# Kernel tuning notes

Measured on AMD Instinct MI355X. Metric: run time of the kernel, lower is better.

Reference implementation:

```python
import jax, jax.numpy as jnp
import numpy as np

B, N, D_IN, D_HID = 8, 2048, 5, 32

def setup_inputs() -> dict:
    key = jax.random.key(0)
    k1, k2, k3, k4 = jax.random.split(key, 4)
    s = jax.random.normal(k1, (B, N, D_IN), dtype=jnp.float32)
    Gmat = jax.random.uniform(k2, (B, N, N), dtype=jnp.float32)
    Qweight = jax.random.normal(k3, (D_IN, D_HID), dtype=jnp.float32)
    Kweight = jax.random.normal(k4, (D_IN, D_HID), dtype=jnp.float32)
    return {"s": s, "Gmat": Gmat, "Qweight": Qweight, "Kweight": Kweight}

def reference(s, Gmat, Qweight, Kweight):
    # s: [B, N, 5]; Gmat: [B, N, N] (or [N, N], broadcastable)
    if Gmat.ndim == 2:
        Gmat = Gmat[None]
    q = jnp.einsum('bnd,dm->bnm', s, Qweight)   # [B, N, 32]
    k = jnp.einsum('bnd,dm->bnm', s, Kweight)   # [B, N, 32]
    att = jnp.square(jnp.einsum('bnm,bjm->bnj', q, k)) * Gmat  # [B, N, N]
    att = att / (jnp.sum(att, axis=2, keepdims=True) + 0.001)
    return att
```

## Files before the change

kernel.cpp:

```cpp
#include <hip/hip_runtime.h>

constexpr int Bc   = 8;
constexpr int Nc   = 2048;
constexpr int DIN  = 5;
constexpr int DHID = 32;

typedef float vf4 __attribute__((ext_vector_type(4)));

__global__ __launch_bounds__(256) void u_precompute(
    const float* __restrict__ s, const float* __restrict__ Qw,
    const float* __restrict__ Kw, float* __restrict__ u)
{
    __shared__ float Msh[DIN * DIN];
    const int tid = threadIdx.x;
    if (tid < DIN * DIN) {
        const int d = tid / DIN, e = tid % DIN;
        float acc = 0.f;
        #pragma unroll
        for (int m = 0; m < DHID; ++m)
            acc = fmaf(Qw[d * DHID + m], Kw[e * DHID + m], acc);
        Msh[tid] = acc;
    }
    __syncthreads();
    const int g = blockIdx.x * 256 + tid;
    if (g >= Bc * Nc) return;
    const int b = g >> 11;
    const int j = g & (Nc - 1);
    float sv[DIN];
    #pragma unroll
    for (int e = 0; e < DIN; ++e) sv[e] = s[(size_t)g * DIN + e];
    #pragma unroll
    for (int d = 0; d < DIN; ++d) {
        float acc = 0.f;
        #pragma unroll
        for (int e = 0; e < DIN; ++e) acc = fmaf(Msh[d * DIN + e], sv[e], acc);
        u[((size_t)b * DIN + d) * Nc + j] = acc;
    }
}

__global__ __launch_bounds__(256) void att_wave_row(
    const float* __restrict__ s, const float* __restrict__ G,
    const float* __restrict__ u, float* __restrict__ out, long gbs)
{
    const int tid  = threadIdx.x;
    const int lane = tid & 63;
    const int wid  = tid >> 6;
    const int row  = blockIdx.x * 4 + wid;
    const int b    = row >> 11;
    const int i    = row & (Nc - 1);

    const float* gRow = G + (size_t)b * gbs + (size_t)i * Nc;
    const float* ub   = u + (size_t)b * DIN * Nc;
    float*       oRow = out + (size_t)row * Nc;

    float si[DIN];
    #pragma unroll
    for (int d = 0; d < DIN; ++d) si[d] = s[(size_t)row * DIN + d];

    float4 g4[8];
    #pragma unroll
    for (int k = 0; k < 8; ++k)
        g4[k] = *reinterpret_cast<const float4*>(gRow + k * 256 + lane * 4);

    float a[8][4];
    float psum = 0.f;
    #pragma unroll
    for (int k = 0; k < 8; ++k) {
        const int j0 = k * 256 + lane * 4;
        float vx = 0.f, vy = 0.f, vz = 0.f, vw = 0.f;
        #pragma unroll
        for (int d = 0; d < DIN; ++d) {
            const float4 u4 = *reinterpret_cast<const float4*>(ub + (size_t)d * Nc + j0);
            vx = fmaf(si[d], u4.x, vx);
            vy = fmaf(si[d], u4.y, vy);
            vz = fmaf(si[d], u4.z, vz);
            vw = fmaf(si[d], u4.w, vw);
        }
        a[k][0] = vx * vx * g4[k].x;
        a[k][1] = vy * vy * g4[k].y;
        a[k][2] = vz * vz * g4[k].z;
        a[k][3] = vw * vw * g4[k].w;
        psum += (a[k][0] + a[k][1]) + (a[k][2] + a[k][3]);
    }

    #pragma unroll
    for (int off = 32; off > 0; off >>= 1)
        psum += __shfl_xor(psum, off, 64);
    const float inv = 1.0f / (psum + 0.001f);

    #pragma unroll
    for (int k = 0; k < 8; ++k) {
        const int j0 = k * 256 + lane * 4;
        vf4 o;
        o.x = a[k][0] * inv;
        o.y = a[k][1] * inv;
        o.z = a[k][2] * inv;
        o.w = a[k][3] * inv;
        __builtin_nontemporal_store(o, reinterpret_cast<vf4*>(oRow + j0));
    }
}

__global__ __launch_bounds__(256) void att_row_direct(
    const float* __restrict__ s, const float* __restrict__ G,
    const float* __restrict__ Qw, const float* __restrict__ Kw,
    float* __restrict__ out, long gbs)
{
    __shared__ float Msh[DIN * DIN];
    __shared__ float wpart[4];
    const int tid = threadIdx.x;
    if (tid < DIN * DIN) {
        const int d = tid / DIN, e = tid % DIN;
        float acc = 0.f;
        #pragma unroll
        for (int m = 0; m < DHID; ++m)
            acc = fmaf(Qw[d * DHID + m], Kw[e * DHID + m], acc);
        Msh[tid] = acc;
    }
    __syncthreads();

    const int row = blockIdx.x;
    const int b   = row >> 11;
    const int i   = row & (Nc - 1);

    float w[DIN];
    {
        float si[DIN];
        #pragma unroll
        for (int e = 0; e < DIN; ++e) si[e] = s[(size_t)row * DIN + e];
        #pragma unroll
        for (int d = 0; d < DIN; ++d) {
            float acc = 0.f;
            #pragma unroll
            for (int e = 0; e < DIN; ++e) acc = fmaf(si[e], Msh[e * DIN + d], acc);
            w[d] = acc;
        }
    }

    const float* gRow = G + (size_t)b * gbs + (size_t)i * Nc;
    const float* sb   = s + (size_t)b * Nc * DIN;
    float*       oRow = out + (size_t)row * Nc;

    float a[2][4];
    float lsum = 0.f;
    #pragma unroll
    for (int it = 0; it < 2; ++it) {
        const int j0 = it * 1024 + tid * 4;
        const float4 g4 = *reinterpret_cast<const float4*>(gRow + j0);
        float v[4];
        #pragma unroll
        for (int c = 0; c < 4; ++c) {
            const float* sj = sb + (size_t)(j0 + c) * DIN;
            float acc = 0.f;
            #pragma unroll
            for (int d = 0; d < DIN; ++d) acc = fmaf(w[d], sj[d], acc);
            v[c] = acc;
        }
        a[it][0] = v[0] * v[0] * g4.x;
        a[it][1] = v[1] * v[1] * g4.y;
        a[it][2] = v[2] * v[2] * g4.z;
        a[it][3] = v[3] * v[3] * g4.w;
        lsum += (a[it][0] + a[it][1]) + (a[it][2] + a[it][3]);
    }

    #pragma unroll
    for (int off = 32; off > 0; off >>= 1)
        lsum += __shfl_xor(lsum, off, 64);
    if ((tid & 63) == 0) wpart[tid >> 6] = lsum;
    __syncthreads();
    const float total = (wpart[0] + wpart[1]) + (wpart[2] + wpart[3]);
    const float inv = 1.0f / (total + 0.001f);

    #pragma unroll
    for (int it = 0; it < 2; ++it) {
        const int j0 = it * 1024 + tid * 4;
        vf4 o;
        o.x = a[it][0] * inv;
        o.y = a[it][1] * inv;
        o.z = a[it][2] * inv;
        o.w = a[it][3] * inv;
        __builtin_nontemporal_store(o, reinterpret_cast<vf4*>(oRow + j0));
    }
}

extern "C" void kernel_launch(void* const* d_in, const int* in_sizes, int n_in,
                              void* d_out, int out_size, void* d_ws, size_t ws_size,
                              hipStream_t stream)
{
    const float* s  = (const float*)d_in[0];
    const float* G  = (const float*)d_in[1];
    const float* Qw = (const float*)d_in[2];
    const float* Kw = (const float*)d_in[3];
    float* out = (float*)d_out;

    const long gbs = (in_sizes[1] == Nc * Nc) ? 0L : (long)Nc * Nc;

    const size_t uBytes = (size_t)Bc * DIN * Nc * sizeof(float);
    if (ws_size >= uBytes) {
        float* u = (float*)d_ws;
        u_precompute<<<(Bc * Nc + 255) / 256, 256, 0, stream>>>(s, Qw, Kw, u);
        att_wave_row<<<(Bc * Nc) / 4, 256, 0, stream>>>(s, G, u, out, gbs);
    } else {
        att_row_direct<<<Bc * Nc, 256, 0, stream>>>(s, G, Qw, Kw, out, gbs);
    }
}
```

Before: 251.6 us.

## Split row normalization into atomic-sum pass and separate grid-stride write pass

Replaces the one-wave-per-row fused kernel with two grid-stride kernels. The first accumulates per-row sums via wave reductions and atomicAdd into a zeroed workspace. The second recomputes attention values and scales them by the inverse sum. This removes the per-thread register arrays and improves occupancy, but G is now read twice and a zeroing kernel plus atomics are added.

New measurement: 291.1 us. 1.16x slower.

```diff
diff --git a/kernel.cpp b/kernel.cpp
--- a/kernel.cpp
+++ b/kernel.cpp
@@ -1,9 +1,11 @@
 #include <hip/hip_runtime.h>
 
-constexpr int Bc   = 8;
-constexpr int Nc   = 2048;
-constexpr int DIN  = 5;
-constexpr int DHID = 32;
+constexpr int  Bc    = 8;
+constexpr int  Nc    = 2048;
+constexpr int  DIN   = 5;
+constexpr int  DHID  = 32;
+constexpr int  NROWS = Bc * Nc;
+constexpr long NF4   = (long)Bc * Nc * (Nc / 4);
 
 typedef float vf4 __attribute__((ext_vector_type(4)));
 
@@ -23,7 +25,7 @@
     }
     __syncthreads();
     const int g = blockIdx.x * 256 + tid;
-    if (g >= Bc * Nc) return;
+    if (g >= NROWS) return;
     const int b = g >> 11;
     const int j = g & (Nc - 1);
     float sv[DIN];
@@ -38,65 +40,82 @@
     }
 }
 
-__global__ __launch_bounds__(256) void att_wave_row(
+__global__ __launch_bounds__(256) void zero_sums(float* __restrict__ sums)
+{
+    const int i = blockIdx.x * 256 + threadIdx.x;
+    if (i < NROWS) sums[i] = 0.f;
+}
+
+__global__ __launch_bounds__(256) void pass1_sums(
     const float* __restrict__ s, const float* __restrict__ G,
-    const float* __restrict__ u, float* __restrict__ out, long gbs)
-{
-    const int tid  = threadIdx.x;
-    const int lane = tid & 63;
-    const int wid  = tid >> 6;
-    const int row  = blockIdx.x * 4 + wid;
-    const int b    = row >> 11;
-    const int i    = row & (Nc - 1);
-
-    const float* gRow = G + (size_t)b * gbs + (size_t)i * Nc;
-    const float* ub   = u + (size_t)b * DIN * Nc;
-    float*       oRow = out + (size_t)row * Nc;
-
-    float si[DIN];
-    #pragma unroll
-    for (int d = 0; d < DIN; ++d) si[d] = s[(size_t)row * DIN + d];
-
-    float4 g4[8];
-    #pragma unroll
-    for (int k = 0; k < 8; ++k)
-        g4[k] = *reinterpret_cast<const float4*>(gRow + k * 256 + lane * 4);
-
-    float a[8][4];
-    float psum = 0.f;
-    #pragma unroll
-    for (int k = 0; k < 8; ++k) {
-        const int j0 = k * 256 + lane * 4;
+    const float* __restrict__ u, float* __restrict__ sums, long gbs)
+{
+    const long stride = (long)gridDim.x * 256;
+    const int  lane   = threadIdx.x & 63;
+    for (long f = (long)blockIdx.x * 256 + threadIdx.x; f < NF4; f += stride) {
+        const int r  = (int)(f >> 9);
+        const int b  = r >> 11;
+        const int i  = r & (Nc - 1);
+        const int j0 = ((int)f & 511) * 4;
+
+        const float4 g4 = *reinterpret_cast<const float4*>(
+            G + (size_t)b * gbs + (size_t)i * Nc + j0);
+
+        const float* sp = s + (size_t)r * DIN;
+        const float* ub = u + (size_t)b * DIN * Nc;
         float vx = 0.f, vy = 0.f, vz = 0.f, vw = 0.f;
         #pragma unroll
         for (int d = 0; d < DIN; ++d) {
+            const float sd = sp[d];
             const float4 u4 = *reinterpret_cast<const float4*>(ub + (size_t)d * Nc + j0);
-            vx = fmaf(si[d], u4.x, vx);
-            vy = fmaf(si[d], u4.y, vy);
-            vz = fmaf(si[d], u4.z, vz);
-            vw = fmaf(si[d], u4.w, vw);
-        }
-        a[k][0] = vx * vx * g4[k].x;
-        a[k][1] = vy * vy * g4[k].y;
-        a[k][2] = vz * vz * g4[k].z;
-        a[k][3] = vw * vw * g4[k].w;
-        psum += (a[k][0] + a[k][1]) + (a[k][2] + a[k][3]);
-    }
-
-    #pragma unroll
-    for (int off = 32; off > 0; off >>= 1)
-        psum += __shfl_xor(psum, off, 64);
-    const float inv = 1.0f / (psum + 0.001f);
-
-    #pragma unroll
-    for (int k = 0; k < 8; ++k) {
-        const int j0 = k * 256 + lane * 4;
+            vx = fmaf(sd, u4.x, vx);
+            vy = fmaf(sd, u4.y, vy);
+            vz = fmaf(sd, u4.z, vz);
+            vw = fmaf(sd, u4.w, vw);
+        }
+        float p = vx * vx * g4.x + vy * vy * g4.y + vz * vz * g4.z + vw * vw * g4.w;
+
+        #pragma unroll
+        for (int off = 32; off > 0; off >>= 1)
+            p += __shfl_xor(p, off, 64);
+        if (lane == 0) atomicAdd(&sums[r], p);
+    }
+}
+
+__global__ __launch_bounds__(256) void pass2_write(
+    const float* __restrict__ s, const float* __restrict__ G,
+    const float* __restrict__ u, const float* __restrict__ sums,
+    float* __restrict__ out, long gbs)
+{
+    const long stride = (long)gridDim.x * 256;
+    for (long f = (long)blockIdx.x * 256 + threadIdx.x; f < NF4; f += stride) {
+        const int r  = (int)(f >> 9);
+        const int b  = r >> 11;
+        const int i  = r & (Nc - 1);
+        const int j0 = ((int)f & 511) * 4;
+
+        const float4 g4 = *reinterpret_cast<const float4*>(
+            G + (size_t)b * gbs + (size_t)i * Nc + j0);
+
+        const float* sp = s + (size_t)r * DIN;
+        const float* ub = u + (size_t)b * DIN * Nc;
+        float vx = 0.f, vy = 0.f, vz = 0.f, vw = 0.f;
+        #pragma unroll
+        for (int d = 0; d < DIN; ++d) {
+            const float sd = sp[d];
+            const float4 u4 = *reinterpret_cast<const float4*>(ub + (size_t)d * Nc + j0);
+            vx = fmaf(sd, u4.x, vx);
+            vy = fmaf(sd, u4.y, vy);
+            vz = fmaf(sd, u4.z, vz);
+            vw = fmaf(sd, u4.w, vw);
+        }
+        const float inv = 1.0f / (sums[r] + 0.001f);
         vf4 o;
-        o.x = a[k][0] * inv;
-        o.y = a[k][1] * inv;
-        o.z = a[k][2] * inv;
-        o.w = a[k][3] * inv;
-        __builtin_nontemporal_store(o, reinterpret_cast<vf4*>(oRow + j0));
+        o.x = vx * vx * g4.x * inv;
+        o.y = vy * vy * g4.y * inv;
+        o.z = vz * vz * g4.z * inv;
+        o.w = vw * vw * g4.w * inv;
+        __builtin_nontemporal_store(o, reinterpret_cast<vf4*>(out + (f << 2)));
     }
 }
 
@@ -194,12 +213,18 @@
 
     const long gbs = (in_sizes[1] == Nc * Nc) ? 0L : (long)Nc * Nc;
 
-    const size_t uBytes = (size_t)Bc * DIN * Nc * sizeof(float);
-    if (ws_size >= uBytes) {
-        float* u = (float*)d_ws;
-        u_precompute<<<(Bc * Nc + 255) / 256, 256, 0, stream>>>(s, Qw, Kw, u);
-        att_wave_row<<<(Bc * Nc) / 4, 256, 0, stream>>>(s, G, u, out, gbs);
+    const size_t sumBytes = (size_t)NROWS * sizeof(float);
+    const size_t uBytes   = (size_t)Bc * DIN * Nc * sizeof(float);
+
+    if (ws_size >= sumBytes + uBytes) {
+        float* sums = (float*)d_ws;
+        float* u    = sums + NROWS;
+
+        zero_sums<<<(NROWS + 255) / 256, 256, 0, stream>>>(sums);
+        u_precompute<<<(NROWS + 255) / 256, 256, 0, stream>>>(s, Qw, Kw, u);
+        pass1_sums<<<2048, 256, 0, stream>>>(s, G, u, sums, gbs);
+        pass2_write<<<2048, 256, 0, stream>>>(s, G, u, sums, out, gbs);
     } else {
-        att_row_direct<<<Bc * Nc, 256, 0, stream>>>(s, G, Qw, Kw, out, gbs);
-    }
-}
+        att_row_direct<<<NROWS, 256, 0, stream>>>(s, G, Qw, Kw, out, gbs);
+    }
+}
```
